# Performance work log

Measured on AMD Instinct MI355X. Metric: run time of the kernel, lower is better.

The kernel has to match this reference:

```python
import jax, jax.numpy as jnp
import numpy as np

N, E, G = 100000, 1600000, 5000
F_IN, H = 128, 3
C1, C2, C3 = 64, 32, 16
SLOPE = 0.2


def _gat_conv(x, W, a_src, a_dst, b, src, dst, n_nodes, heads, ch):
    # x: [N, F_in] -> h: [N, H, C]
    h = (x @ W).reshape(n_nodes, heads, ch)
    alpha_s = jnp.sum(h * a_src, axis=-1)  # [N, H]
    alpha_d = jnp.sum(h * a_dst, axis=-1)  # [N, H]
    e = jax.nn.leaky_relu(alpha_s[src] + alpha_d[dst], SLOPE)  # [E, H]
    # segment softmax over destination nodes (numerically stable)
    e_max = jax.ops.segment_max(e, dst, num_segments=n_nodes)
    e_max = jnp.where(jnp.isfinite(e_max), e_max, 0.0)
    ex = jnp.exp(e - e_max[dst])
    denom = jax.ops.segment_sum(ex, dst, num_segments=n_nodes)
    alpha = ex / (denom[dst] + 1e-16)  # [E, H]
    msg = h[src] * alpha[:, :, None]  # [E, H, C]
    out = jax.ops.segment_sum(msg, dst, num_segments=n_nodes)  # [N, H, C]
    return out.reshape(n_nodes, heads * ch) + b


def setup_inputs() -> dict:
    key = jax.random.key(0)
    ks = jax.random.split(key, 20)
    def w(k, shape, fan_in):
        return jax.random.normal(k, shape, jnp.float32) / np.sqrt(fan_in)
    return {
        "x": jax.random.normal(ks[0], (N, F_IN), jnp.float32),
        "y": jax.random.uniform(ks[1], (G,), jnp.float32),
        "edge_index": jax.random.randint(ks[2], (2, E), 0, N, jnp.int32),
        "batch": jnp.sort(jax.random.randint(ks[3], (N,), 0, G, jnp.int32)),
        "W1": w(ks[4], (F_IN, H * C1), F_IN),
        "as1": w(ks[5], (H, C1), C1),
        "ad1": w(ks[6], (H, C1), C1),
        "b1": jnp.zeros((H * C1,), jnp.float32),
        "W2": w(ks[7], (H * C1, H * C2), H * C1),
        "as2": w(ks[8], (H, C2), C2),
        "ad2": w(ks[9], (H, C2), C2),
        "b2": jnp.zeros((H * C2,), jnp.float32),
        "W3": w(ks[10], (H * C2, H * C3), H * C2),
        "as3": w(ks[11], (H, C3), C3),
        "ad3": w(ks[12], (H, C3), C3),
        "b3": jnp.zeros((H * C3,), jnp.float32),
        "Wl": w(ks[13], (H * C3, 1), H * C3),
        "bl": jnp.zeros((1,), jnp.float32),
    }


def reference(x, y, edge_index, batch, W1, as1, ad1, b1, W2, as2, ad2, b2,
              W3, as3, ad3, b3, Wl, bl):
    n = x.shape[0]
    loops = jnp.arange(n, dtype=edge_index.dtype)
    src = jnp.concatenate([edge_index[0], loops])  # PyG add_self_loops=True
    dst = jnp.concatenate([edge_index[1], loops])

    h = _gat_conv(x, W1, as1, ad1, b1, src, dst, n, H, C1)
    h = jax.nn.elu(h)
    h = _gat_conv(h, W2, as2, ad2, b2, src, dst, n, H, C2)
    h = jax.nn.elu(h)
    h = _gat_conv(h, W3, as3, ad3, b3, src, dst, n, H, C3)

    # global mean pool over graphs
    counts = jax.ops.segment_sum(jnp.ones((n,), h.dtype), batch, num_segments=G)
    pooled = jax.ops.segment_sum(h, batch, num_segments=G) / jnp.maximum(counts, 1.0)[:, None]
    pooled = jax.nn.relu(pooled)

    logits = pooled @ Wl + bl  # [G, 1]
    t = y.reshape(-1, 1)
    loss = jnp.mean(jax.nn.softplus(logits) - t * logits)  # BCEWithLogits
    out = jax.nn.sigmoid(logits)
    return out, loss
```

## Files before the change

kernel.cpp:

```cpp
#include <hip/hip_runtime.h>
#include <hip/hip_bf16.h>

#define THREADS 256
typedef __hip_bfloat16 bf16;

typedef __bf16 v8bf __attribute__((ext_vector_type(8)));
typedef float  v4f  __attribute__((ext_vector_type(4)));
typedef unsigned int v2u __attribute__((ext_vector_type(2)));

__device__ __forceinline__ float bfl(unsigned u){ return __uint_as_float(u << 16); }
__device__ __forceinline__ float bfh(unsigned u){ return __uint_as_float(u & 0xffff0000u); }

__global__ void hist_k(const int* __restrict__ ei, int* __restrict__ cnt,
                       int* __restrict__ rank, int E, int ET){
  int i = blockIdx.x*THREADS + threadIdx.x;
  if (i >= ET) return;
  int d = (i < E) ? ei[E + i] : (i - E);
  rank[i] = atomicAdd(&cnt[d], 1);
}

__global__ void scan1_k(const int* __restrict__ deg, int* __restrict__ off,
                        int* __restrict__ bsum, int n){
  __shared__ int sh[1024];
  int i = blockIdx.x*1024 + threadIdx.x;
  int v = (i < n) ? deg[i] : 0;
  sh[threadIdx.x] = v;
  __syncthreads();
  for (int s = 1; s < 1024; s <<= 1){
    int t = (threadIdx.x >= s) ? sh[threadIdx.x - s] : 0;
    __syncthreads();
    sh[threadIdx.x] += t;
    __syncthreads();
  }
  if (i < n) off[i+1] = sh[threadIdx.x];
  if (threadIdx.x == 1023) bsum[blockIdx.x] = sh[1023];
}

__global__ void scan2_k(int* __restrict__ bsum, int nb){
  __shared__ int sh[256];
  int v = (threadIdx.x < nb) ? bsum[threadIdx.x] : 0;
  sh[threadIdx.x] = v;
  __syncthreads();
  for (int s = 1; s < 256; s <<= 1){
    int t = (threadIdx.x >= s) ? sh[threadIdx.x - s] : 0;
    __syncthreads();
    sh[threadIdx.x] += t;
    __syncthreads();
  }
  if (threadIdx.x < nb) bsum[threadIdx.x] = sh[threadIdx.x] - v;
}

__global__ void scan3_k(int* __restrict__ off, const int* __restrict__ bsum, int n){
  int i = blockIdx.x*1024 + threadIdx.x;
  if (i < n) off[i+1] += bsum[blockIdx.x];
  if (i == 0) off[0] = 0;
}

__global__ void scatter_k(const int* __restrict__ ei, const int* __restrict__ off,
                          const int* __restrict__ rank, int* __restrict__ csr,
                          int E, int ET){
  int i = blockIdx.x*THREADS + threadIdx.x;
  if (i >= ET) return;
  int s, d;
  if (i < E){ s = ei[i]; d = ei[E+i]; } else { s = i - E; d = i - E; }
  csr[off[d] + rank[i]] = s;
}

__device__ __forceinline__ void wt_do(const float* __restrict__ W, bf16* __restrict__ WT,
                                      int K, int COUT, int i){
  int k = i / COUT, c = i - k*COUT;
  WT[(size_t)c*K + k] = __float2bfloat16(W[i]);
}

__device__ __forceinline__ void va_do(const float* __restrict__ W, const float* __restrict__ as,
                                      const float* __restrict__ ad, bf16* __restrict__ WTX,
                                      int K, int C, int COUT, int i){
  int k = i % K, c6 = i / K;
  int h = (c6 < 3) ? c6 : c6 - 3;
  const float* a = ((c6 < 3) ? as : ad) + h*C;
  const float* wp = W + (size_t)k*COUT + h*C;
  float s = 0.f;
  for (int cc = 0; cc < C; cc++) s += wp[cc]*a[cc];
  WTX[(size_t)(COUT + c6)*K + k] = __float2bfloat16(s);
}

__global__ void prep_k(const float* __restrict__ W1, const float* __restrict__ as1, const float* __restrict__ ad1,
                       const float* __restrict__ W2, const float* __restrict__ as2, const float* __restrict__ ad2,
                       const float* __restrict__ W3, const float* __restrict__ as3, const float* __restrict__ ad3,
                       bf16* __restrict__ WT1, bf16* __restrict__ WT2, bf16* __restrict__ WT3,
                       const int* __restrict__ batch, int* __restrict__ goff, int n, int G)
{
  int i = blockIdx.x*THREADS + threadIdx.x;
  if (i < 24576){ wt_do(W1, WT1, 128, 192, i); return; } i -= 24576;
  if (i < 18432){ wt_do(W2, WT2, 192, 96, i); return; }  i -= 18432;
  if (i < 4608) { wt_do(W3, WT3, 96, 48, i); return; }   i -= 4608;
  if (i < 768)  { va_do(W1, as1, ad1, WT1, 128, 64, 192, i); return; } i -= 768;
  if (i < 1152) { va_do(W2, as2, ad2, WT2, 192, 32, 96, i); return; }  i -= 1152;
  if (i < 576)  { va_do(W3, as3, ad3, WT3, 96, 16, 48, i); return; }   i -= 576;
  if (i <= G){
    if (i == G){ goff[G] = n; return; }
    int lo = 0, hi = n;
    while (lo < hi){ int mid = (lo + hi) >> 1; if (batch[mid] < i) lo = mid + 1; else hi = mid; }
    goff[i] = lo;
  }
}

template<int K, int COUT, bool CVT>
__global__ void __launch_bounds__(256) gemm_mfma_k(
    const void* __restrict__ Av, const bf16* __restrict__ BT,
    bf16* __restrict__ C, float* __restrict__ aS4, float* __restrict__ aD4,
    int nRowTiles)
{
  int wave = threadIdx.x >> 6, lane = threadIdx.x & 63;
  int rt = blockIdx.x*4 + wave;
  if (rt >= nRowTiles) return;
  int half = lane & 15;
  int quad = lane >> 4;
  v8bf aF[K/32];
  if constexpr (CVT){
    const float* aBase = (const float*)Av + (size_t)(rt*16 + half)*K + quad*8;
    #pragma unroll
    for (int kk = 0; kk < K/32; kk++){
      float4 f0 = *(const float4*)(aBase + kk*32);
      float4 f1 = *(const float4*)(aBase + kk*32 + 4);
      v8bf t;
      t[0] = (__bf16)f0.x; t[1] = (__bf16)f0.y; t[2] = (__bf16)f0.z; t[3] = (__bf16)f0.w;
      t[4] = (__bf16)f1.x; t[5] = (__bf16)f1.y; t[6] = (__bf16)f1.z; t[7] = (__bf16)f1.w;
      aF[kk] = t;
    }
  } else {
    const __bf16* aBase = (const __bf16*)Av + (size_t)(rt*16 + half)*K + quad*8;
    #pragma unroll
    for (int kk = 0; kk < K/32; kk++) aF[kk] = *(const v8bf*)(aBase + kk*32);
  }
  #pragma unroll
  for (int cb = 0; cb < COUT + 16; cb += 16){
    const __bf16* bBase = (const __bf16*)BT + (size_t)(cb + half)*K + quad*8;
    v4f acc = {0.f, 0.f, 0.f, 0.f};
    #pragma unroll
    for (int kk = 0; kk < K/32; kk++)
      acc = __builtin_amdgcn_mfma_f32_16x16x32_bf16(aF[kk], *(const v8bf*)(bBase + kk*32), acc, 0, 0, 0);
    int orow = rt*16 + quad*4;
    if (cb < COUT){
      bf16* cp = C + (size_t)orow*COUT + cb + half;
      #pragma unroll
      for (int r = 0; r < 4; r++)
        cp[(size_t)r*COUT] = __float2bfloat16(acc[r]);
    } else if (half < 6){
      #pragma unroll
      for (int r = 0; r < 4; r++){
        int row = orow + r;
        if (half < 3) aS4[row*4 + half]     = acc[r];
        else          aD4[row*4 + half - 3] = acc[r];
      }
    }
  }
}

template<int HC, int CSH, int GRP>
__global__ void __launch_bounds__(256) agg_k(
    const int* __restrict__ off, const int* __restrict__ csr,
    const bf16* __restrict__ hbuf,
    const float* __restrict__ aS4, const float* __restrict__ aD4,
    const float* __restrict__ bias,
    float* __restrict__ outF, bf16* __restrict__ outB,
    int n, int doElu)
{
  constexpr int NPW = 64 / GRP;
  __shared__ __align__(16) float wls[4][384];
  int tid = threadIdx.x;
  int wave = tid >> 6;
  int lane = tid & 63;
  int q = lane % GRP;
  int grp = lane / GRP;
  const int hq = (4*q) >> CSH;
  const bool act = q < HC/4;
  const unsigned q8 = 8u*q;
  float* gbase = &wls[wave][grp*3*GRP*2];
  const float* wh = gbase + hq*GRP*2;
  const char* hb = (const char*)hbuf;
  float4 bv = {0.f, 0.f, 0.f, 0.f};
  if (act) bv = *(const float4*)(bias + 4*q);

  int nodeTot = (n + NPW - 1) / NPW;
  int nwv = gridDim.x * 4;
  for (int wv = (blockIdx.x*256 + tid) >> 6; wv < nodeTot; wv += nwv){
    int node = wv*NPW + grp;
    bool valid = node < n;
    int e0 = 0, e1 = 0;
    float4 ad = {0.f, 0.f, 0.f, 0.f};
    if (valid){
      e0 = off[node]; e1 = off[node+1];
      ad = *(const float4*)(aD4 + 4*node);
    }
    float dh = 0.f;
    float a0 = 0.f, a1 = 0.f, a2 = 0.f, a3 = 0.f;

    int nch = (e1 - e0 + GRP - 1) / GRP;
    for (int c = 0; c < nch; c++){
      int base = e0 + c*GRP;
      __threadfence_block();
      int j = base + q;
      if (j < e1){
        int s = __builtin_nontemporal_load(&csr[j]);
        float4 av = *(const float4*)(aS4 + 4*s);
        float x0 = av.x + ad.x; x0 = (x0 > 0.f) ? x0 : 0.2f*x0;
        float x1 = av.y + ad.y; x1 = (x1 > 0.f) ? x1 : 0.2f*x1;
        float x2 = av.z + ad.z; x2 = (x2 > 0.f) ? x2 : 0.2f*x2;
        float sf = __int_as_float(s * (HC*2));
        float2 p0 = {__expf(x0), sf};
        float2 p1 = {__expf(x1), sf};
        float2 p2 = {__expf(x2), sf};
        *(float2*)(gbase + (0*GRP + q)*2) = p0;
        *(float2*)(gbase + (1*GRP + q)*2) = p1;
        *(float2*)(gbase + (2*GRP + q)*2) = p2;
      }
      __threadfence_block();
      if (act){
        int lim = e1 - base; if (lim > GRP) lim = GRP;
        int jj = 0;
        for (; jj + 8 <= lim; jj += 8){
          float4 pA = *(const float4*)(wh + jj*2);
          float4 pB = *(const float4*)(wh + jj*2 + 4);
          float4 pC = *(const float4*)(wh + jj*2 + 8);
          float4 pD = *(const float4*)(wh + jj*2 + 12);
          unsigned o0 = __float_as_uint(pA.y) + q8, o1 = __float_as_uint(pA.w) + q8;
          unsigned o2 = __float_as_uint(pB.y) + q8, o3 = __float_as_uint(pB.w) + q8;
          unsigned o4 = __float_as_uint(pC.y) + q8, o5 = __float_as_uint(pC.w) + q8;
          unsigned o6 = __float_as_uint(pD.y) + q8, o7 = __float_as_uint(pD.w) + q8;
          float w0 = pA.x, w1 = pA.z, w2 = pB.x, w3 = pB.z;
          float w4 = pC.x, w5 = pC.z, w6 = pD.x, w7 = pD.z;
          uint2 u0 = *(const uint2*)(hb + o0);
          uint2 u1 = *(const uint2*)(hb + o1);
          uint2 u2 = *(const uint2*)(hb + o2);
          uint2 u3 = *(const uint2*)(hb + o3);
          uint2 u4 = *(const uint2*)(hb + o4);
          uint2 u5 = *(const uint2*)(hb + o5);
          uint2 u6 = *(const uint2*)(hb + o6);
          uint2 u7 = *(const uint2*)(hb + o7);
          dh += w0 + w1 + w2 + w3 + w4 + w5 + w6 + w7;
          a0 += w0*bfl(u0.x); a1 += w0*bfh(u0.x); a2 += w0*bfl(u0.y); a3 += w0*bfh(u0.y);
          a0 += w1*bfl(u1.x); a1 += w1*bfh(u1.x); a2 += w1*bfl(u1.y); a3 += w1*bfh(u1.y);
          a0 += w2*bfl(u2.x); a1 += w2*bfh(u2.x); a2 += w2*bfl(u2.y); a3 += w2*bfh(u2.y);
          a0 += w3*bfl(u3.x); a1 += w3*bfh(u3.x); a2 += w3*bfl(u3.y); a3 += w3*bfh(u3.y);
          a0 += w4*bfl(u4.x); a1 += w4*bfh(u4.x); a2 += w4*bfl(u4.y); a3 += w4*bfh(u4.y);
          a0 += w5*bfl(u5.x); a1 += w5*bfh(u5.x); a2 += w5*bfl(u5.y); a3 += w5*bfh(u5.y);
          a0 += w6*bfl(u6.x); a1 += w6*bfh(u6.x); a2 += w6*bfl(u6.y); a3 += w6*bfh(u6.y);
          a0 += w7*bfl(u7.x); a1 += w7*bfh(u7.x); a2 += w7*bfl(u7.y); a3 += w7*bfh(u7.y);
        }
        for (; jj + 4 <= lim; jj += 4){
          float4 pA = *(const float4*)(wh + jj*2);
          float4 pB = *(const float4*)(wh + jj*2 + 4);
          unsigned o0 = __float_as_uint(pA.y) + q8, o1 = __float_as_uint(pA.w) + q8;
          unsigned o2 = __float_as_uint(pB.y) + q8, o3 = __float_as_uint(pB.w) + q8;
          float w0 = pA.x, w1 = pA.z, w2 = pB.x, w3 = pB.z;
          uint2 u0 = *(const uint2*)(hb + o0);
          uint2 u1 = *(const uint2*)(hb + o1);
          uint2 u2 = *(const uint2*)(hb + o2);
          uint2 u3 = *(const uint2*)(hb + o3);
          dh += w0 + w1 + w2 + w3;
          a0 += w0*bfl(u0.x); a1 += w0*bfh(u0.x); a2 += w0*bfl(u0.y); a3 += w0*bfh(u0.y);
          a0 += w1*bfl(u1.x); a1 += w1*bfh(u1.x); a2 += w1*bfl(u1.y); a3 += w1*bfh(u1.y);
          a0 += w2*bfl(u2.x); a1 += w2*bfh(u2.x); a2 += w2*bfl(u2.y); a3 += w2*bfh(u2.y);
          a0 += w3*bfl(u3.x); a1 += w3*bfh(u3.x); a2 += w3*bfl(u3.y); a3 += w3*bfh(u3.y);
        }
        for (; jj < lim; jj++){
          float2 pw = *(const float2*)(wh + jj*2);
          unsigned o = __float_as_uint(pw.y) + q8;
          float w = pw.x;
          uint2 u = *(const uint2*)(hb + o);
          dh += w;
          a0 += w*bfl(u.x); a1 += w*bfh(u.x); a2 += w*bfl(u.y); a3 += w*bfh(u.y);
        }
      }
    }
    if (act && valid){
      float inv = 1.f / (dh + 1e-16f);
      float r0 = a0*inv + bv.x, r1 = a1*inv + bv.y, r2 = a2*inv + bv.z, r3 = a3*inv + bv.w;
      if (doElu){
        r0 = (r0 > 0.f) ? r0 : (__expf(r0) - 1.f);
        r1 = (r1 > 0.f) ? r1 : (__expf(r1) - 1.f);
        r2 = (r2 > 0.f) ? r2 : (__expf(r2) - 1.f);
        r3 = (r3 > 0.f) ? r3 : (__expf(r3) - 1.f);
      }
      if (outF){
        v4f o = {r0, r1, r2, r3};
        __builtin_nontemporal_store(o, (v4f*)(outF + (size_t)node*HC + 4*q));
      }
      if (outB){
        union { bf16 h[4]; v2u u; } cv;
        cv.h[0] = __float2bfloat16(r0); cv.h[1] = __float2bfloat16(r1);
        cv.h[2] = __float2bfloat16(r2); cv.h[3] = __float2bfloat16(r3);
        __builtin_nontemporal_store(cv.u, (v2u*)(outB + (size_t)node*HC + 4*q));
      }
    }
  }
}

__global__ void __launch_bounds__(256) pool_logits_k(
    const float* __restrict__ h3, const int* __restrict__ goff,
    const float* __restrict__ Wl, const float* __restrict__ bl,
    const float* __restrict__ y, float* __restrict__ outp,
    float* __restrict__ lossAcc, int G)
{
  int lane = threadIdx.x & 63;
  int g = (blockIdx.x*256 + threadIdx.x) >> 6;
  if (g >= G) return;
  int n0 = goff[g], n1 = goff[g+1];
  int cnt = n1 - n0;
  float acc = 0.f, acc2 = 0.f, wl = 0.f;
  if (lane < 48){
    wl = Wl[lane];
    const float* p = h3 + (size_t)n0*48 + lane;
    int i = 0;
    for (; i + 2 <= cnt; i += 2){ acc += p[(size_t)i*48]; acc2 += p[(size_t)(i+1)*48]; }
    if (i < cnt) acc += p[(size_t)i*48];
    acc += acc2;
  }
  float inv = 1.f / fmaxf((float)cnt, 1.f);
  float v = fmaxf(acc*inv, 0.f) * wl;
  for (int o = 32; o > 0; o >>= 1) v += __shfl_down(v, o);
  if (lane == 0){
    float logit = v + bl[0];
    outp[g] = 1.f / (1.f + __expf(-logit));
    float t = y[g];
    float sp = (logit > 0.f) ? (logit + log1pf(__expf(-logit))) : log1pf(__expf(logit));
    atomicAdd(lossAcc, sp - t*logit);
  }
}

__global__ void fin_k(const float* __restrict__ lossAcc, float* __restrict__ outp, int gtot){
  outp[gtot] = lossAcc[0] / (float)gtot;
}

extern "C" void kernel_launch(void* const* d_in, const int* in_sizes, int n_in,
                              void* d_out, int out_size, void* d_ws, size_t ws_size,
                              hipStream_t stream)
{
  (void)n_in; (void)out_size; (void)ws_size;
  const float* x    = (const float*)d_in[0];
  const float* y    = (const float*)d_in[1];
  const int*  ei    = (const int*)d_in[2];
  const int*  batch = (const int*)d_in[3];
  const float* W1 = (const float*)d_in[4];
  const float* as1= (const float*)d_in[5];
  const float* ad1= (const float*)d_in[6];
  const float* b1 = (const float*)d_in[7];
  const float* W2 = (const float*)d_in[8];
  const float* as2= (const float*)d_in[9];
  const float* ad2= (const float*)d_in[10];
  const float* b2 = (const float*)d_in[11];
  const float* W3 = (const float*)d_in[12];
  const float* as3= (const float*)d_in[13];
  const float* ad3= (const float*)d_in[14];
  const float* b3 = (const float*)d_in[15];
  const float* Wl = (const float*)d_in[16];
  const float* bl = (const float*)d_in[17];
  float* outp = (float*)d_out;

  int Nn = in_sizes[0] / 128;
  int Gg = in_sizes[1];
  int Ee = in_sizes[2] / 2;
  int ET = Ee + Nn;

  char* p = (char*)d_ws;
  auto carve = [&](size_t bytes) -> void* {
    void* r = (void*)p; p += (bytes + 255) & ~(size_t)255; return r;
  };
  int*   off     = (int*)  carve((size_t)(Nn+1)*4);
  int*   cnt     = (int*)  carve((size_t)Nn*4);
  int*   csr     = (int*)  carve((size_t)ET*4);
  int*   rank    = (int*)  carve((size_t)ET*4);
  int*   bsum    = (int*)  carve(256*4);
  float* aS4     = (float*)carve((size_t)Nn*4*4);
  float* aD4     = (float*)carve((size_t)Nn*4*4);
  int*   goff    = (int*)  carve((size_t)(Gg+1)*4);
  float* lossAcc = (float*)carve(4);
  bf16*  WT1     = (bf16*) carve((size_t)(192+16)*128*2);
  bf16*  WT2     = (bf16*) carve((size_t)(96+16)*192*2);
  bf16*  WT3     = (bf16*) carve((size_t)(48+16)*96*2);
  bf16*  bufH    = (bf16*) carve((size_t)Nn*192*2);
  bf16*  bufA    = (bf16*) carve((size_t)Nn*192*2);
  float* bufO    = (float*)((char*)bufH + ((size_t)Nn*96 + 255 & ~(size_t)255));

  int NB = (Nn + 1023) / 1024;
  int ebk = (ET + THREADS - 1) / THREADS;

  hipMemsetAsync(cnt, 0, (size_t)Nn*4, stream);
  hist_k<<<ebk, THREADS, 0, stream>>>(ei, cnt, rank, Ee, ET);
  scan1_k<<<NB, 1024, 0, stream>>>(cnt, off, bsum, Nn);
  scan2_k<<<1, 256, 0, stream>>>(bsum, NB);
  scan3_k<<<NB, 1024, 0, stream>>>(off, bsum, Nn);
  scatter_k<<<ebk, THREADS, 0, stream>>>(ei, off, rank, csr, Ee, ET);

  int prepTot = 24576 + 18432 + 4608 + 768 + 1152 + 576 + (Gg + 1);
  prep_k<<<(prepTot + THREADS-1)/THREADS, THREADS, 0, stream>>>(
      W1, as1, ad1, W2, as2, ad2, W3, as3, ad3, WT1, WT2, WT3, batch, goff, Nn, Gg);

  int nRT = Nn / 16;
  int gx  = (nRT + 3) / 4;
  int aggGrid = 2048;

  gemm_mfma_k<128,192,true><<<gx, 256, 0, stream>>>(x, WT1, bufH, aS4, aD4, nRT);
  agg_k<192,6,64><<<aggGrid, 256, 0, stream>>>(off, csr, bufH, aS4, aD4, b1, nullptr, bufA, Nn, 1);
  gemm_mfma_k<192,96,false><<<gx, 256, 0, stream>>>(bufA, WT2, bufH, aS4, aD4, nRT);
  agg_k<96,5,32><<<aggGrid, 256, 0, stream>>>(off, csr, bufH, aS4, aD4, b2, nullptr, bufA, Nn, 1);
  gemm_mfma_k<96,48,false><<<gx, 256, 0, stream>>>(bufA, WT3, bufH, aS4, aD4, nRT);
  agg_k<48,4,16><<<aggGrid, 256, 0, stream>>>(off, csr, bufH, aS4, aD4, b3, bufO, nullptr, Nn, 0);

  hipMemsetAsync(lossAcc, 0, 4, stream);
  pool_logits_k<<<(Gg + 3)/4, 256, 0, stream>>>(bufO, goff, Wl, bl, y, outp, lossAcc, Gg);
  fin_k<<<1, 1, 0, stream>>>(lossAcc, outp, Gg);
}
```

Baseline: 655.2 us.

## Widen aggregation gathers to 8 channels per lane and launch one wave per node group

Each active lane in the GAT aggregation kernel now gathers 16-byte (8 bf16) feature chunks per neighbour instead of 8-byte chunks, so half as many lanes issue twice-as-wide loads. The persistent grid-stride loop over node groups is replaced by a grid sized so each wave handles exactly one node group. The 8-edge unrolled inner loop becomes 4/2/1 unrolls, and nontemporal loads and stores become plain accesses. This aims to cut gather instruction count and loop overhead, but it leaves more lanes idle per wave and launches many more blocks.

```diff
diff --git a/kernel.cpp b/kernel.cpp
--- a/kernel.cpp
+++ b/kernel.cpp
@@ -6,7 +6,6 @@
 
 typedef __bf16 v8bf __attribute__((ext_vector_type(8)));
 typedef float  v4f  __attribute__((ext_vector_type(4)));
-typedef unsigned int v2u __attribute__((ext_vector_type(2)));
 
 __device__ __forceinline__ float bfl(unsigned u){ return __uint_as_float(u << 16); }
 __device__ __forceinline__ float bfh(unsigned u){ return __uint_as_float(u & 0xffff0000u); }
@@ -167,132 +166,125 @@
     int n, int doElu)
 {
   constexpr int NPW = 64 / GRP;
+  constexpr int AL  = HC / 8;
   __shared__ __align__(16) float wls[4][384];
   int tid = threadIdx.x;
   int wave = tid >> 6;
   int lane = tid & 63;
   int q = lane % GRP;
   int grp = lane / GRP;
-  const int hq = (4*q) >> CSH;
-  const bool act = q < HC/4;
-  const unsigned q8 = 8u*q;
+  int wv = (blockIdx.x*256 + tid) >> 6;
+  int node = wv*NPW + grp;
+  bool valid = node < n;
+  int e0 = 0, e1 = 0;
+  float4 ad = {0.f, 0.f, 0.f, 0.f};
+  if (valid){
+    e0 = off[node]; e1 = off[node+1];
+    ad = *(const float4*)(aD4 + 4*node);
+  }
+  const int hq = (8*q) >> CSH;
+  const bool act = valid && (q < AL);
+  const unsigned q16 = 16u*q;
+  float dh = 0.f;
+  float a0 = 0.f, a1 = 0.f, a2 = 0.f, a3 = 0.f;
+  float a4 = 0.f, a5 = 0.f, a6 = 0.f, a7 = 0.f;
   float* gbase = &wls[wave][grp*3*GRP*2];
   const float* wh = gbase + hq*GRP*2;
   const char* hb = (const char*)hbuf;
-  float4 bv = {0.f, 0.f, 0.f, 0.f};
-  if (act) bv = *(const float4*)(bias + 4*q);
-
-  int nodeTot = (n + NPW - 1) / NPW;
-  int nwv = gridDim.x * 4;
-  for (int wv = (blockIdx.x*256 + tid) >> 6; wv < nodeTot; wv += nwv){
-    int node = wv*NPW + grp;
-    bool valid = node < n;
-    int e0 = 0, e1 = 0;
-    float4 ad = {0.f, 0.f, 0.f, 0.f};
-    if (valid){
-      e0 = off[node]; e1 = off[node+1];
-      ad = *(const float4*)(aD4 + 4*node);
-    }
-    float dh = 0.f;
-    float a0 = 0.f, a1 = 0.f, a2 = 0.f, a3 = 0.f;
-
-    int nch = (e1 - e0 + GRP - 1) / GRP;
-    for (int c = 0; c < nch; c++){
-      int base = e0 + c*GRP;
-      __threadfence_block();
-      int j = base + q;
-      if (j < e1){
-        int s = __builtin_nontemporal_load(&csr[j]);
-        float4 av = *(const float4*)(aS4 + 4*s);
-        float x0 = av.x + ad.x; x0 = (x0 > 0.f) ? x0 : 0.2f*x0;
-        float x1 = av.y + ad.y; x1 = (x1 > 0.f) ? x1 : 0.2f*x1;
-        float x2 = av.z + ad.z; x2 = (x2 > 0.f) ? x2 : 0.2f*x2;
-        float sf = __int_as_float(s * (HC*2));
-        float2 p0 = {__expf(x0), sf};
-        float2 p1 = {__expf(x1), sf};
-        float2 p2 = {__expf(x2), sf};
-        *(float2*)(gbase + (0*GRP + q)*2) = p0;
-        *(float2*)(gbase + (1*GRP + q)*2) = p1;
-        *(float2*)(gbase + (2*GRP + q)*2) = p2;
+
+#define ACC8(U,W) \
+  a0 += (W)*bfl((U).x); a1 += (W)*bfh((U).x); a2 += (W)*bfl((U).y); a3 += (W)*bfh((U).y); \
+  a4 += (W)*bfl((U).z); a5 += (W)*bfh((U).z); a6 += (W)*bfl((U).w); a7 += (W)*bfh((U).w);
+
+  int nch = (e1 - e0 + GRP - 1) / GRP;
+  for (int c = 0; c < nch; c++){
+    int base = e0 + c*GRP;
+    __threadfence_block();
+    int j = base + q;
+    if (j < e1){
+      int s = csr[j];
+      float4 av = *(const float4*)(aS4 + 4*s);
+      float x0 = av.x + ad.x; x0 = (x0 > 0.f) ? x0 : 0.2f*x0;
+      float x1 = av.y + ad.y; x1 = (x1 > 0.f) ? x1 : 0.2f*x1;
+      float x2 = av.z + ad.z; x2 = (x2 > 0.f) ? x2 : 0.2f*x2;
+      float sf = __int_as_float(s * (HC*2));
+      float2 p0 = {__expf(x0), sf};
+      float2 p1 = {__expf(x1), sf};
+      float2 p2 = {__expf(x2), sf};
+      *(float2*)(gbase + (0*GRP + q)*2) = p0;
+      *(float2*)(gbase + (1*GRP + q)*2) = p1;
+      *(float2*)(gbase + (2*GRP + q)*2) = p2;
+    }
+    __threadfence_block();
+    if (act){
+      int lim = e1 - base; if (lim > GRP) lim = GRP;
+      int jj = 0;
+      for (; jj + 4 <= lim; jj += 4){
+        float4 pA = *(const float4*)(wh + jj*2);
+        float4 pB = *(const float4*)(wh + jj*2 + 4);
+        unsigned o0 = __float_as_uint(pA.y) + q16, o1 = __float_as_uint(pA.w) + q16;
+        unsigned o2 = __float_as_uint(pB.y) + q16, o3 = __float_as_uint(pB.w) + q16;
+        float w0 = pA.x, w1 = pA.z, w2 = pB.x, w3 = pB.z;
+        uint4 u0 = *(const uint4*)(hb + o0);
+        uint4 u1 = *(const uint4*)(hb + o1);
+        uint4 u2 = *(const uint4*)(hb + o2);
+        uint4 u3 = *(const uint4*)(hb + o3);
+        dh += w0 + w1 + w2 + w3;
+        ACC8(u0, w0);
+        ACC8(u1, w1);
+        ACC8(u2, w2);
+        ACC8(u3, w3);
       }
-      __threadfence_block();
-      if (act){
-        int lim = e1 - base; if (lim > GRP) lim = GRP;
-        int jj = 0;
-        for (; jj + 8 <= lim; jj += 8){
-          float4 pA = *(const float4*)(wh + jj*2);
-          float4 pB = *(const float4*)(wh + jj*2 + 4);
-          float4 pC = *(const float4*)(wh + jj*2 + 8);
-          float4 pD = *(const float4*)(wh + jj*2 + 12);
-          unsigned o0 = __float_as_uint(pA.y) + q8, o1 = __float_as_uint(pA.w) + q8;
-          unsigned o2 = __float_as_uint(pB.y) + q8, o3 = __float_as_uint(pB.w) + q8;
-          unsigned o4 = __float_as_uint(pC.y) + q8, o5 = __float_as_uint(pC.w) + q8;
-          unsigned o6 = __float_as_uint(pD.y) + q8, o7 = __float_as_uint(pD.w) + q8;
-          float w0 = pA.x, w1 = pA.z, w2 = pB.x, w3 = pB.z;
-          float w4 = pC.x, w5 = pC.z, w6 = pD.x, w7 = pD.z;
-          uint2 u0 = *(const uint2*)(hb + o0);
-          uint2 u1 = *(const uint2*)(hb + o1);
-          uint2 u2 = *(const uint2*)(hb + o2);
-          uint2 u3 = *(const uint2*)(hb + o3);
-          uint2 u4 = *(const uint2*)(hb + o4);
-          uint2 u5 = *(const uint2*)(hb + o5);
-          uint2 u6 = *(const uint2*)(hb + o6);
-          uint2 u7 = *(const uint2*)(hb + o7);
-          dh += w0 + w1 + w2 + w3 + w4 + w5 + w6 + w7;
-          a0 += w0*bfl(u0.x); a1 += w0*bfh(u0.x); a2 += w0*bfl(u0.y); a3 += w0*bfh(u0.y);
-          a0 += w1*bfl(u1.x); a1 += w1*bfh(u1.x); a2 += w1*bfl(u1.y); a3 += w1*bfh(u1.y);
-          a0 += w2*bfl(u2.x); a1 += w2*bfh(u2.x); a2 += w2*bfl(u2.y); a3 += w2*bfh(u2.y);
-          a0 += w3*bfl(u3.x); a1 += w3*bfh(u3.x); a2 += w3*bfl(u3.y); a3 += w3*bfh(u3.y);
-          a0 += w4*bfl(u4.x); a1 += w4*bfh(u4.x); a2 += w4*bfl(u4.y); a3 += w4*bfh(u4.y);
-          a0 += w5*bfl(u5.x); a1 += w5*bfh(u5.x); a2 += w5*bfl(u5.y); a3 += w5*bfh(u5.y);
-          a0 += w6*bfl(u6.x); a1 += w6*bfh(u6.x); a2 += w6*bfl(u6.y); a3 += w6*bfh(u6.y);
-          a0 += w7*bfl(u7.x); a1 += w7*bfh(u7.x); a2 += w7*bfl(u7.y); a3 += w7*bfh(u7.y);
-        }
-        for (; jj + 4 <= lim; jj += 4){
-          float4 pA = *(const float4*)(wh + jj*2);
-          float4 pB = *(const float4*)(wh + jj*2 + 4);
-          unsigned o0 = __float_as_uint(pA.y) + q8, o1 = __float_as_uint(pA.w) + q8;
-          unsigned o2 = __float_as_uint(pB.y) + q8, o3 = __float_as_uint(pB.w) + q8;
-          float w0 = pA.x, w1 = pA.z, w2 = pB.x, w3 = pB.z;
-          uint2 u0 = *(const uint2*)(hb + o0);
-          uint2 u1 = *(const uint2*)(hb + o1);
-          uint2 u2 = *(const uint2*)(hb + o2);
-          uint2 u3 = *(const uint2*)(hb + o3);
-          dh += w0 + w1 + w2 + w3;
-          a0 += w0*bfl(u0.x); a1 += w0*bfh(u0.x); a2 += w0*bfl(u0.y); a3 += w0*bfh(u0.y);
-          a0 += w1*bfl(u1.x); a1 += w1*bfh(u1.x); a2 += w1*bfl(u1.y); a3 += w1*bfh(u1.y);
-          a0 += w2*bfl(u2.x); a1 += w2*bfh(u2.x); a2 += w2*bfl(u2.y); a3 += w2*bfh(u2.y);
-          a0 += w3*bfl(u3.x); a1 += w3*bfh(u3.x); a2 += w3*bfl(u3.y); a3 += w3*bfh(u3.y);
-        }
-        for (; jj < lim; jj++){
-          float2 pw = *(const float2*)(wh + jj*2);
-          unsigned o = __float_as_uint(pw.y) + q8;
-          float w = pw.x;
-          uint2 u = *(const uint2*)(hb + o);
-          dh += w;
-          a0 += w*bfl(u.x); a1 += w*bfh(u.x); a2 += w*bfl(u.y); a3 += w*bfh(u.y);
-        }
+      for (; jj + 2 <= lim; jj += 2){
+        float4 pA = *(const float4*)(wh + jj*2);
+        unsigned o0 = __float_as_uint(pA.y) + q16, o1 = __float_as_uint(pA.w) + q16;
+        float w0 = pA.x, w1 = pA.z;
+        uint4 u0 = *(const uint4*)(hb + o0);
+        uint4 u1 = *(const uint4*)(hb + o1);
+        dh += w0 + w1;
+        ACC8(u0, w0);
+        ACC8(u1, w1);
       }
-    }
-    if (act && valid){
-      float inv = 1.f / (dh + 1e-16f);
-      float r0 = a0*inv + bv.x, r1 = a1*inv + bv.y, r2 = a2*inv + bv.z, r3 = a3*inv + bv.w;
-      if (doElu){
-        r0 = (r0 > 0.f) ? r0 : (__expf(r0) - 1.f);
-        r1 = (r1 > 0.f) ? r1 : (__expf(r1) - 1.f);
-        r2 = (r2 > 0.f) ? r2 : (__expf(r2) - 1.f);
-        r3 = (r3 > 0.f) ? r3 : (__expf(r3) - 1.f);
+      for (; jj < lim; jj++){
+        float2 pw = *(const float2*)(wh + jj*2);
+        unsigned o = __float_as_uint(pw.y) + q16;
+        float w = pw.x;
+        uint4 u = *(const uint4*)(hb + o);
+        dh += w;
+        ACC8(u, w);
       }
-      if (outF){
-        v4f o = {r0, r1, r2, r3};
-        __builtin_nontemporal_store(o, (v4f*)(outF + (size_t)node*HC + 4*q));
-      }
-      if (outB){
-        union { bf16 h[4]; v2u u; } cv;
-        cv.h[0] = __float2bfloat16(r0); cv.h[1] = __float2bfloat16(r1);
-        cv.h[2] = __float2bfloat16(r2); cv.h[3] = __float2bfloat16(r3);
-        __builtin_nontemporal_store(cv.u, (v2u*)(outB + (size_t)node*HC + 4*q));
-      }
+    }
+  }
+#undef ACC8
+  if (act){
+    float inv = 1.f / (dh + 1e-16f);
+    const float4 bA = *(const float4*)(bias + 8*q);
+    const float4 bB = *(const float4*)(bias + 8*q + 4);
+    float r0 = a0*inv + bA.x, r1 = a1*inv + bA.y, r2 = a2*inv + bA.z, r3 = a3*inv + bA.w;
+    float r4 = a4*inv + bB.x, r5 = a5*inv + bB.y, r6 = a6*inv + bB.z, r7 = a7*inv + bB.w;
+    if (doElu){
+      r0 = (r0 > 0.f) ? r0 : (__expf(r0) - 1.f);
+      r1 = (r1 > 0.f) ? r1 : (__expf(r1) - 1.f);
+      r2 = (r2 > 0.f) ? r2 : (__expf(r2) - 1.f);
+      r3 = (r3 > 0.f) ? r3 : (__expf(r3) - 1.f);
+      r4 = (r4 > 0.f) ? r4 : (__expf(r4) - 1.f);
+      r5 = (r5 > 0.f) ? r5 : (__expf(r5) - 1.f);
+      r6 = (r6 > 0.f) ? r6 : (__expf(r6) - 1.f);
+      r7 = (r7 > 0.f) ? r7 : (__expf(r7) - 1.f);
+    }
+    if (outF){
+      float4 oA = {r0, r1, r2, r3};
+      float4 oB = {r4, r5, r6, r7};
+      *(float4*)(outF + (size_t)node*HC + 8*q)     = oA;
+      *(float4*)(outF + (size_t)node*HC + 8*q + 4) = oB;
+    }
+    if (outB){
+      union { bf16 h[8]; uint4 u; } cv;
+      cv.h[0] = __float2bfloat16(r0); cv.h[1] = __float2bfloat16(r1);
+      cv.h[2] = __float2bfloat16(r2); cv.h[3] = __float2bfloat16(r3);
+      cv.h[4] = __float2bfloat16(r4); cv.h[5] = __float2bfloat16(r5);
+      cv.h[6] = __float2bfloat16(r6); cv.h[7] = __float2bfloat16(r7);
+      *(uint4*)(outB + (size_t)node*HC + 8*q) = cv.u;
     }
   }
 }
@@ -399,14 +391,16 @@
 
   int nRT = Nn / 16;
   int gx  = (nRT + 3) / 4;
-  int aggGrid = 2048;
+  int gb1 = (Nn + 3) / 4;
+  int gb2 = (Nn + 7) / 8;
+  int gb3 = (Nn + 15) / 16;
 
   gemm_mfma_k<128,192,true><<<gx, 256, 0, stream>>>(x, WT1, bufH, aS4, aD4, nRT);
-  agg_k<192,6,64><<<aggGrid, 256, 0, stream>>>(off, csr, bufH, aS4, aD4, b1, nullptr, bufA, Nn, 1);
+  agg_k<192,6,64><<<gb1, 256, 0, stream>>>(off, csr, bufH, aS4, aD4, b1, nullptr, bufA, Nn, 1);
   gemm_mfma_k<192,96,false><<<gx, 256, 0, stream>>>(bufA, WT2, bufH, aS4, aD4, nRT);
-  agg_k<96,5,32><<<aggGrid, 256, 0, stream>>>(off, csr, bufH, aS4, aD4, b2, nullptr, bufA, Nn, 1);
+  agg_k<96,5,32><<<gb2, 256, 0, stream>>>(off, csr, bufH, aS4, aD4, b2, nullptr, bufA, Nn, 1);
   gemm_mfma_k<96,48,false><<<gx, 256, 0, stream>>>(bufA, WT3, bufH, aS4, aD4, nRT);
-  agg_k<48,4,16><<<aggGrid, 256, 0, stream>>>(off, csr, bufH, aS4, aD4, b3, bufO, nullptr, Nn, 0);
+  agg_k<48,4,16><<<gb3, 256, 0, stream>>>(off, csr, bufH, aS4, aD4, b3, bufO, nullptr, Nn, 0);
 
   hipMemsetAsync(lossAcc, 0, 4, stream);
   pool_logits_k<<<(Gg + 3)/4, 256, 0, stream>>>(bufO, goff, Wl, bl, y, outp, lossAcc, Gg);
```

Measured after the change: 615.3 us (median of 2 runs). 1.06x faster.
